# Optimization experiments

Hardware: AMD Instinct MI355X
Metric: run time of the kernel (lower is better)

The kernel has to match this reference:

```python
import jax, jax.numpy as jnp
import numpy as np

# Faithful, vectorized JAX version of Warpformer.hour_aggregate from SQHyper/Warpformer.
# Original loops over time_split=range(new_l+1) building per-bin masks and doing
# max_pool1d / masked sums; here we collapse that into segment reductions keyed by
# bin = floor(event_time) (since bins are [i, i+1)).


def setup_inputs() -> dict:
    key = jax.random.key(0)
    k1, k2, k3 = jax.random.split(key, 3)
    B, K, L, D = 16, 32, 1024, 128
    NEW_L = 48
    h0 = jax.random.normal(k1, (B, K, L, D), dtype=jnp.float32)
    # event times uniformly spread over the [0, NEW_L) window
    event_time = jax.random.uniform(k2, (B, L), dtype=jnp.float32) * NEW_L
    non_pad_mask = (jax.random.uniform(k3, (B, K, L)) > 0.1).astype(jnp.float32)
    return {"h0": h0, "event_time": event_time, "non_pad_mask": non_pad_mask, "new_l": NEW_L}


def reference(h0, event_time, non_pad_mask, new_l):
    b, k, l, d = h0.shape
    ns = new_l + 1  # extra dummy segment for out-of-range times
    valid = (event_time >= 0) & (event_time < new_l)
    seg = jnp.where(valid, jnp.floor(event_time).astype(jnp.int32), new_l)  # [b,l]

    def per_batch(h, et, npm, s):
        # h: [k,l,d], et: [l], npm: [k,l], s: [l]
        h_lkd = jnp.transpose(h, (1, 0, 2))                                   # [l,k,d]
        segmax = jax.ops.segment_max(h_lkd, s, num_segments=ns)               # [ns,k,d]
        counts = jax.ops.segment_sum(jnp.ones_like(et), s, num_segments=ns)   # [ns]
        tsum = jax.ops.segment_sum(et, s, num_segments=ns)                    # [ns]
        msum = jax.ops.segment_sum(jnp.transpose(npm, (1, 0)), s, num_segments=ns)  # [ns,k]
        return segmax, counts, tsum, msum

    segmax, counts, tsum, msum = jax.vmap(per_batch)(h0, event_time, non_pad_mask, seg)
    segmax = segmax[:, :new_l]   # [b,new_l,k,d]
    counts = counts[:, :new_l]   # [b,new_l]
    tsum = tsum[:, :new_l]
    msum = msum[:, :new_l]       # [b,new_l,k]

    denom = jnp.maximum(counts, 1.0)
    # Original does max_pool1d over h0*mask: zeros participate whenever bin has < l members
    # (empty bins -> 0, partially-filled bins -> max(members, 0)).
    include_zero = counts < l
    new_h0 = jnp.where(include_zero[:, :, None, None], jnp.maximum(segmax, 0.0), segmax)
    new_h0 = jnp.transpose(new_h0, (0, 2, 1, 3))  # [b,k,new_l,d]

    new_event_time = jnp.broadcast_to((tsum / denom)[:, None, :], (b, k, new_l))
    new_pad_mask = jnp.transpose(msum, (0, 2, 1)) / denom[:, None, :]  # [b,k,new_l]

    almat = (seg[:, :, None] == jnp.arange(new_l)[None, None, :]).astype(h0.dtype)  # [b,l,new_l]
    almat = jnp.broadcast_to(almat[:, None], (b, k, l, new_l))
    return new_h0, new_event_time, new_pad_mask, almat
```

## Files before the change

### kernel.cpp

```cpp
#include <hip/hip_runtime.h>
#include <math.h>

constexpr int CB = 16, CK = 32, CL = 1024, CD = 128, CNL = 48;

typedef float f32x4 __attribute__((ext_vector_type(4)));

constexpr size_t OUT_H0 = 0;
constexpr size_t OUT_ET = (size_t)CB * CK * CNL * CD;
constexpr size_t OUT_PM = OUT_ET + (size_t)CB * CK * CNL;
constexpr size_t OUT_AL = OUT_PM + (size_t)CB * CK * CNL;

__device__ __forceinline__ unsigned fmap(float f) {
    int i = __float_as_int(f);
    return (unsigned)(i ^ (int)(0x80000000u | (unsigned)(i >> 31)));
}
__device__ __forceinline__ float funmap(unsigned u) {
    return (u & 0x80000000u) ? __int_as_float((int)(u & 0x7FFFFFFFu))
                             : __int_as_float(~(int)u);
}
#define FMAP_NEG_INF 0x007FFFFFu

__device__ __forceinline__ int swz(int d) { return d ^ (d >> 5); }

__global__ __launch_bounds__(512) void fused_kernel(
    const float* __restrict__ h0, const float* __restrict__ et,
    const float* __restrict__ npm, float* __restrict__ out) {
    __shared__ unsigned acc[(CNL + 1) * CD];
    __shared__ float cnt_s[CNL + 1];
    __shared__ float ts_s[CNL + 1];
    __shared__ float ms_s[CNL + 1];
    __shared__ int segl[CL];

    const int bk = blockIdx.x;
    const int b = bk >> 5;
    const int t = threadIdx.x;

    for (int c = t; c < (CNL + 1) * CD; c += 512) acc[c] = FMAP_NEG_INF;
    if (t < CNL + 1) { cnt_s[t] = 0.f; ts_s[t] = 0.f; ms_s[t] = 0.f; }
    __syncthreads();

    {
        const float2 e2 = ((const float2*)(et + b * CL))[t];
        const float2 m2 = ((const float2*)(npm + (size_t)bk * CL))[t];
        const int l0 = 2 * t;
        bool va = (e2.x >= 0.f) && (e2.x < (float)CNL);
        bool vb = (e2.y >= 0.f) && (e2.y < (float)CNL);
        int sa = va ? (int)e2.x : CNL;
        int sb = vb ? (int)e2.y : CNL;
        segl[l0] = sa;
        segl[l0 + 1] = sb;
        if (va) { atomicAdd(&cnt_s[sa], 1.f); atomicAdd(&ts_s[sa], e2.x); }
        if (vb) { atomicAdd(&cnt_s[sb], 1.f); atomicAdd(&ts_s[sb], e2.y); }
        atomicAdd(&ms_s[sa], m2.x);
        atomicAdd(&ms_s[sb], m2.y);
    }
    __syncthreads();

    {
        f32x4* oa = (f32x4*)(out + OUT_AL + (size_t)bk * CL * CNL);
#pragma unroll
        for (int i = 0; i < 24; ++i) {
            const int idx = t + i * 512;
            const int row = idx / 12;
            const int c4 = idx - row * 12;
            const int s = segl[row];
            const int c = c4 * 4;
            f32x4 v;
            v.x = (c + 0 == s) ? 1.f : 0.f;
            v.y = (c + 1 == s) ? 1.f : 0.f;
            v.z = (c + 2 == s) ? 1.f : 0.f;
            v.w = (c + 3 == s) ? 1.f : 0.f;
            __builtin_nontemporal_store(v, &oa[idx]);
        }
    }

    const float* hb = h0 + (size_t)bk * CL * CD;
    const int rlane = t >> 5;
    const int d4 = (t & 31) * 4;
    const int a0 = swz(d4 + 0);
    const int a1 = swz(d4 + 1);
    const int a2 = swz(d4 + 2);
    const int a3 = swz(d4 + 3);
#pragma unroll 8
    for (int step = 0; step < 64; ++step) {
        const int r = step * 16 + rlane;
        const f32x4 v =
            __builtin_nontemporal_load((const f32x4*)(hb + (size_t)r * CD + d4));
        const int s = segl[r];
        unsigned* arow = &acc[s * CD];
        atomicMax(arow + a0, fmap(v.x));
        atomicMax(arow + a1, fmap(v.y));
        atomicMax(arow + a2, fmap(v.z));
        atomicMax(arow + a3, fmap(v.w));
    }
    __syncthreads();

    float* oh = out + OUT_H0 + (size_t)bk * CNL * CD;
    for (int c = t; c < CNL * CD; c += 512) {
        const int s = c >> 7;
        const int d = c & 127;
        float v = funmap(acc[s * CD + swz(d)]);
        if (cnt_s[s] < (float)CL) v = fmaxf(v, 0.f);
        __builtin_nontemporal_store(v, &oh[c]);
    }
    if (t < CNL) {
        const float den = fmaxf(cnt_s[t], 1.f);
        out[OUT_ET + (size_t)bk * CNL + t] = ts_s[t] / den;
        out[OUT_PM + (size_t)bk * CNL + t] = ms_s[t] / den;
    }
}

extern "C" void kernel_launch(void* const* d_in, const int* in_sizes, int n_in,
                              void* d_out, int out_size, void* d_ws, size_t ws_size,
                              hipStream_t stream) {
    (void)in_sizes; (void)n_in; (void)out_size; (void)d_ws; (void)ws_size;
    const float* h0  = (const float*)d_in[0];
    const float* et  = (const float*)d_in[1];
    const float* npm = (const float*)d_in[2];
    float* out = (float*)d_out;

    fused_kernel<<<CB * CK, 512, 0, stream>>>(h0, et, npm, out);
}
```

Baseline: 382.2 us.

## Replace LDS atomicMax scatter with counting-sort bucketing and per-wave gather max

Rows are bucketed by segment with a counting sort into a shared index list. Each wavefront then walks one segment's rows, loading 2 floats per lane and reducing the max in registers before a single store. This removes the per-element shared-memory atomicMax traffic, the float/uint remapping and the separate readout pass. The cost is a serial prefix scan on one thread, extra barriers, and gathered row loads whose memory parallelism is limited to four loads in flight per wave.

```diff
diff --git a/kernel.cpp b/kernel.cpp
--- a/kernel.cpp
+++ b/kernel.cpp
@@ -4,39 +4,29 @@
 constexpr int CB = 16, CK = 32, CL = 1024, CD = 128, CNL = 48;
 
 typedef float f32x4 __attribute__((ext_vector_type(4)));
+typedef float f32x2 __attribute__((ext_vector_type(2)));
 
 constexpr size_t OUT_H0 = 0;
 constexpr size_t OUT_ET = (size_t)CB * CK * CNL * CD;
 constexpr size_t OUT_PM = OUT_ET + (size_t)CB * CK * CNL;
 constexpr size_t OUT_AL = OUT_PM + (size_t)CB * CK * CNL;
 
-__device__ __forceinline__ unsigned fmap(float f) {
-    int i = __float_as_int(f);
-    return (unsigned)(i ^ (int)(0x80000000u | (unsigned)(i >> 31)));
-}
-__device__ __forceinline__ float funmap(unsigned u) {
-    return (u & 0x80000000u) ? __int_as_float((int)(u & 0x7FFFFFFFu))
-                             : __int_as_float(~(int)u);
-}
-#define FMAP_NEG_INF 0x007FFFFFu
-
-__device__ __forceinline__ int swz(int d) { return d ^ (d >> 5); }
-
 __global__ __launch_bounds__(512) void fused_kernel(
     const float* __restrict__ h0, const float* __restrict__ et,
     const float* __restrict__ npm, float* __restrict__ out) {
-    __shared__ unsigned acc[(CNL + 1) * CD];
-    __shared__ float cnt_s[CNL + 1];
+    __shared__ int segl[CL];
+    __shared__ int list[CL];
+    __shared__ int icnt[CNL + 1];
+    __shared__ int offs[CNL + 2];
+    __shared__ int fill[CNL + 1];
     __shared__ float ts_s[CNL + 1];
     __shared__ float ms_s[CNL + 1];
-    __shared__ int segl[CL];
 
     const int bk = blockIdx.x;
     const int b = bk >> 5;
     const int t = threadIdx.x;
 
-    for (int c = t; c < (CNL + 1) * CD; c += 512) acc[c] = FMAP_NEG_INF;
-    if (t < CNL + 1) { cnt_s[t] = 0.f; ts_s[t] = 0.f; ms_s[t] = 0.f; }
+    if (t < CNL + 1) { icnt[t] = 0; fill[t] = 0; ts_s[t] = 0.f; ms_s[t] = 0.f; }
     __syncthreads();
 
     {
@@ -49,10 +39,29 @@
         int sb = vb ? (int)e2.y : CNL;
         segl[l0] = sa;
         segl[l0 + 1] = sb;
-        if (va) { atomicAdd(&cnt_s[sa], 1.f); atomicAdd(&ts_s[sa], e2.x); }
-        if (vb) { atomicAdd(&cnt_s[sb], 1.f); atomicAdd(&ts_s[sb], e2.y); }
+        atomicAdd(&icnt[sa], 1);
+        atomicAdd(&icnt[sb], 1);
+        if (va) atomicAdd(&ts_s[sa], e2.x);
+        if (vb) atomicAdd(&ts_s[sb], e2.y);
         atomicAdd(&ms_s[sa], m2.x);
         atomicAdd(&ms_s[sb], m2.y);
+    }
+    __syncthreads();
+
+    if (t == 0) {
+        int acc = 0;
+        for (int s = 0; s <= CNL; ++s) { offs[s] = acc; acc += icnt[s]; }
+        offs[CNL + 1] = acc;
+    }
+    __syncthreads();
+
+    {
+        const int l0 = 2 * t;
+        const int sa = segl[l0], sb = segl[l0 + 1];
+        int pa = atomicAdd(&fill[sa], 1);
+        list[offs[sa] + pa] = l0;
+        int pb = atomicAdd(&fill[sb], 1);
+        list[offs[sb] + pb] = l0 + 1;
     }
     __syncthreads();
 
@@ -75,36 +84,47 @@
     }
 
     const float* hb = h0 + (size_t)bk * CL * CD;
-    const int rlane = t >> 5;
-    const int d4 = (t & 31) * 4;
-    const int a0 = swz(d4 + 0);
-    const int a1 = swz(d4 + 1);
-    const int a2 = swz(d4 + 2);
-    const int a3 = swz(d4 + 3);
-#pragma unroll 8
-    for (int step = 0; step < 64; ++step) {
-        const int r = step * 16 + rlane;
-        const f32x4 v =
-            __builtin_nontemporal_load((const f32x4*)(hb + (size_t)r * CD + d4));
-        const int s = segl[r];
-        unsigned* arow = &acc[s * CD];
-        atomicMax(arow + a0, fmap(v.x));
-        atomicMax(arow + a1, fmap(v.y));
-        atomicMax(arow + a2, fmap(v.z));
-        atomicMax(arow + a3, fmap(v.w));
+    float* oh = out + OUT_H0 + (size_t)bk * CNL * CD;
+    const int wid = t >> 6;
+    const int lane = t & 63;
+    const int d0 = lane * 2;
+    for (int s = wid; s < CNL; s += 8) {
+        const int beg = offs[s];
+        const int end = offs[s + 1];
+        float vx = -__builtin_inff(), vy = -__builtin_inff();
+        int i = beg;
+        for (; i + 4 <= end; i += 4) {
+            const int r0 = list[i + 0];
+            const int r1 = list[i + 1];
+            const int r2 = list[i + 2];
+            const int r3 = list[i + 3];
+            const f32x2 v0 = __builtin_nontemporal_load(
+                (const f32x2*)(hb + (size_t)r0 * CD + d0));
+            const f32x2 v1 = __builtin_nontemporal_load(
+                (const f32x2*)(hb + (size_t)r1 * CD + d0));
+            const f32x2 v2 = __builtin_nontemporal_load(
+                (const f32x2*)(hb + (size_t)r2 * CD + d0));
+            const f32x2 v3 = __builtin_nontemporal_load(
+                (const f32x2*)(hb + (size_t)r3 * CD + d0));
+            vx = fmaxf(fmaxf(fmaxf(fmaxf(vx, v0.x), v1.x), v2.x), v3.x);
+            vy = fmaxf(fmaxf(fmaxf(fmaxf(vy, v0.y), v1.y), v2.y), v3.y);
+        }
+        for (; i < end; ++i) {
+            const int r = list[i];
+            const f32x2 v = __builtin_nontemporal_load(
+                (const f32x2*)(hb + (size_t)r * CD + d0));
+            vx = fmaxf(vx, v.x);
+            vy = fmaxf(vy, v.y);
+        }
+        if (end - beg < CL) { vx = fmaxf(vx, 0.f); vy = fmaxf(vy, 0.f); }
+        f32x2 o;
+        o.x = vx;
+        o.y = vy;
+        __builtin_nontemporal_store(o, (f32x2*)(oh + s * CD + d0));
     }
-    __syncthreads();
 
-    float* oh = out + OUT_H0 + (size_t)bk * CNL * CD;
-    for (int c = t; c < CNL * CD; c += 512) {
-        const int s = c >> 7;
-        const int d = c & 127;
-        float v = funmap(acc[s * CD + swz(d)]);
-        if (cnt_s[s] < (float)CL) v = fmaxf(v, 0.f);
-        __builtin_nontemporal_store(v, &oh[c]);
-    }
     if (t < CNL) {
-        const float den = fmaxf(cnt_s[t], 1.f);
+        const float den = fmaxf((float)icnt[t], 1.f);
         out[OUT_ET + (size_t)bk * CNL + t] = ts_s[t] / den;
         out[OUT_PM + (size_t)bk * CNL + t] = ms_s[t] / den;
     }
```

After: 392.2 us. 1.03x slower.
